# Kernel tuning notes

Hardware: AMD Instinct MI355X
Metric: run time of the kernel (lower is better)

Reference implementation:

```python
import jax, jax.numpy as jnp
import numpy as np

_SAMPLING_EPS = 1e-5


def setup_inputs() -> dict:
    key = jax.random.key(0)
    k1, k2, k3, k4, k5 = jax.random.split(key, 5)
    B, V = 128, 128000
    logits = jax.random.normal(k1, (B, V), dtype=jnp.float32)
    temperature = jax.random.uniform(k2, (B,), dtype=jnp.float32)  # some rows < eps -> greedy
    top_k = jax.random.randint(k3, (B,), 1, 64, dtype=jnp.int32)   # in [1, 63]
    top_p = jax.random.uniform(k4, (B,), dtype=jnp.float32, minval=0.05, maxval=1.0)
    noise_u = jax.random.uniform(k5, (B, V), dtype=jnp.float32, minval=1e-10, maxval=1.0)
    return {"logits": logits, "temperature": temperature, "top_k": top_k,
            "top_p": top_p, "noise_u": noise_u, "max_num_logprobs": 5}


def _apply_top_k_top_p(logits, k, p):
    # Faithful to vLLM: ascending sort, top-k threshold mask, top-p cumsum mask, scatter back.
    B, V = logits.shape
    order = jnp.argsort(logits, axis=-1)                       # ascending, [B, V]
    logits_sort = jnp.take_along_axis(logits, order, axis=-1)
    neg_inf = jnp.float32(-jnp.inf)
    # top-k: pivot value at position V - k; everything strictly below it -> -inf
    pivot_idx = (V - k.astype(jnp.int32))[:, None]             # [B, 1]
    pivot = jnp.take_along_axis(logits_sort, pivot_idx, axis=-1)
    logits_sort = jnp.where(logits_sort < pivot, neg_inf, logits_sort)
    # top-p: softmax over sorted logits, cumsum, drop prefix with mass <= 1 - p (keep last)
    probs_sort = jax.nn.softmax(logits_sort, axis=-1)
    probs_sum = jnp.cumsum(probs_sort, axis=-1)
    top_p_mask = probs_sum <= (1.0 - p)[:, None]
    top_p_mask = top_p_mask.at[:, -1].set(False)
    logits_sort = jnp.where(top_p_mask, neg_inf, logits_sort)
    # scatter back to original vocab order
    rows = jnp.arange(B)[:, None]
    return jnp.zeros_like(logits).at[rows, order].set(logits_sort)


def reference(logits, temperature, top_k, top_p, noise_u, max_num_logprobs):
    # temperature scaling (temp < eps means greedy; divide by 1.0 instead)
    temp = jnp.where(temperature < _SAMPLING_EPS, 1.0, temperature)
    logits = logits.astype(jnp.float32) / temp[:, None]
    # top-k / top-p filtering
    logits = _apply_top_k_top_p(logits, top_k, top_p)
    # probabilities and sampling
    probs = jax.nn.softmax(logits, axis=-1)
    greedy = jnp.argmax(probs, axis=-1)
    q = -jnp.log(noise_u)                                      # Exp(1) noise (q.exponential_())
    random = jnp.argmax(probs / q, axis=-1)
    sampled = jnp.where(temperature < _SAMPLING_EPS, greedy, random).astype(jnp.int32)
    # top-k logprobs
    logprobs = jax.nn.log_softmax(logits, axis=-1)
    topk_logprobs, topk_indices = jax.lax.top_k(logprobs, max_num_logprobs)
    return sampled, topk_indices.astype(jnp.int32), topk_logprobs
```

## Files before the change

### kernel.cpp

```cpp
#include <hip/hip_runtime.h>
#include <math.h>
#include <stdint.h>

#define BT     256
#define WPB    4
#define TOPC   64
#define CAPW   1024
#define WT     512
#define NSL_HI 16
#define NSL_LO 8
#define NC_MAX (NSL_HI * TOPC)

__device__ __forceinline__ unsigned f2ord(float f) {
    unsigned u = __float_as_uint(f);
    return u ^ ((u & 0x80000000u) ? 0xFFFFFFFFu : 0x80000000u);
}
__device__ __forceinline__ float ord2f(unsigned k) {
    unsigned u = (k & 0x80000000u) ? (k ^ 0x80000000u) : (k ^ 0xFFFFFFFFu);
    return __uint_as_float(u);
}

__device__ unsigned wave_rebuild64(unsigned* key, int* idx, unsigned n,
                                   int lane, unsigned* out_vst)
{
    unsigned kr[16]; int ir[16];
    #pragma unroll
    for (int g = 0; g < 16; ++g) {
        unsigned i = (unsigned)(g * 64 + lane);
        kr[g] = (i < n) ? key[i] : 0u;
        ir[g] = (i < n) ? idx[i] : 0;
    }
    unsigned p = 0u;
    for (int bit = 31; bit >= 0; --bit) {
        unsigned t = p | (1u << bit);
        int c = 0;
        #pragma unroll
        for (int g = 0; g < 16; ++g)
            c += __popcll(__ballot(kr[g] >= t));
        if (c >= TOPC) p = t;
    }
    const unsigned long long ltm = (1ull << lane) - 1ull;
    unsigned c = 0;
    #pragma unroll
    for (int g = 0; g < 16; ++g) {
        unsigned i = (unsigned)(g * 64 + lane);
        bool pa = (i < n) && (kr[g] > p);
        unsigned long long m = __ballot(pa);
        if (pa) { unsigned pos = c + (unsigned)__popcll(m & ltm); key[pos] = kr[g]; idx[pos] = ir[g]; }
        c += (unsigned)__popcll(m);
    }
    #pragma unroll
    for (int g = 0; g < 16; ++g) {
        unsigned i = (unsigned)(g * 64 + lane);
        bool pa = (i < n) && (kr[g] == p);
        unsigned long long m = __ballot(pa);
        if (pa) {
            unsigned pos = c + (unsigned)__popcll(m & ltm);
            if (pos < TOPC) { key[pos] = kr[g]; idx[pos] = ir[g]; }
        }
        c += (unsigned)__popcll(m);
    }
    *out_vst = p;
    return (c < TOPC) ? c : TOPC;
}

__global__ __launch_bounds__(BT) void phase1_topk_slices(
    const float* __restrict__ logits, uint2* __restrict__ cand,
    int V, int slice_len, int nsl)
{
    __shared__ unsigned s_key[WPB][CAPW];
    __shared__ int      s_idx[WPB][CAPW];

    const int row  = blockIdx.y;
    const int tid  = threadIdx.x;
    const int wid  = tid >> 6;
    const int lane = tid & 63;
    const int sl   = blockIdx.x * WPB + wid;
    const int s0   = sl * slice_len;
    int s_end = s0 + slice_len; if (s_end > V) s_end = V;
    const float* rowp = logits + (size_t)row * (size_t)V;
    unsigned* mykey = s_key[wid];
    int*      myidx = s_idx[wid];
    const unsigned long long ltm = (1ull << lane) - 1ull;

    const int  tb0 = s0 + lane * 8, tb1 = s0 + WT + lane * 8;
    const bool vt0 = tb0 < s_end,   vt1 = tb1 < s_end;
    float4 sa0 = {}, sb0 = {}, sa1 = {}, sb1 = {};
    if (vt0) { sa0 = *(const float4*)(rowp + tb0); sb0 = *(const float4*)(rowp + tb0 + 4); }
    if (vt1) { sa1 = *(const float4*)(rowp + tb1); sb1 = *(const float4*)(rowp + tb1 + 4); }

    const int t2 = s0 + 2 * WT, t3 = s0 + 3 * WT;
    const int pb0 = t2 + lane * 8, pb1 = t3 + lane * 8;
    bool pv0 = pb0 < s_end, pv1 = pb1 < s_end;
    float4 A0 = {}, B0 = {}, A1 = {}, B1 = {};
    if (pv0) { A0 = *(const float4*)(rowp + pb0); B0 = *(const float4*)(rowp + pb0 + 4); }
    if (pv1) { A1 = *(const float4*)(rowp + pb1); B1 = *(const float4*)(rowp + pb1 + 4); }

    unsigned k0[8], k1[8];
    if (vt0) {
        k0[0] = f2ord(sa0.x); k0[1] = f2ord(sa0.y); k0[2] = f2ord(sa0.z); k0[3] = f2ord(sa0.w);
        k0[4] = f2ord(sb0.x); k0[5] = f2ord(sb0.y); k0[6] = f2ord(sb0.z); k0[7] = f2ord(sb0.w);
    } else {
        #pragma unroll
        for (int j = 0; j < 8; ++j) k0[j] = 0u;
    }
    if (vt1) {
        k1[0] = f2ord(sa1.x); k1[1] = f2ord(sa1.y); k1[2] = f2ord(sa1.z); k1[3] = f2ord(sa1.w);
        k1[4] = f2ord(sb1.x); k1[5] = f2ord(sb1.y); k1[6] = f2ord(sb1.z); k1[7] = f2ord(sb1.w);
    } else {
        #pragma unroll
        for (int j = 0; j < 8; ++j) k1[j] = 0u;
    }

    unsigned lo = 0u, hi = 0xFFFFu;
    while (lo < hi) {
        unsigned mid = (lo + hi + 1u) >> 1;
        unsigned t = mid << 16;
        int cnt16 = 0;
        #pragma unroll
        for (int j = 0; j < 8; ++j) {
            cnt16 += __popcll(__ballot(k0[j] >= t));
            cnt16 += __popcll(__ballot(k1[j] >= t));
        }
        if (cnt16 >= TOPC) lo = mid; else hi = mid - 1u;
    }
    const unsigned thr = lo << 16;

    unsigned cnt = 0u;
    auto append8 = [&](const unsigned* k, int base, bool valid) {
        #pragma unroll
        for (int j = 0; j < 8; ++j) {
            bool pa = valid && (k[j] >= thr);
            unsigned long long m = __ballot(pa);
            if (pa) {
                unsigned pos = cnt + (unsigned)__popcll(m & ltm);
                if (pos < CAPW) { mykey[pos] = k[j]; myidx[pos] = base + j; }
            }
            cnt += (unsigned)__popcll(m);
        }
    };
    auto conv8 = [&](unsigned* k, const float4& a, const float4& b, bool valid) {
        if (valid) {
            k[0] = f2ord(a.x); k[1] = f2ord(a.y); k[2] = f2ord(a.z); k[3] = f2ord(a.w);
            k[4] = f2ord(b.x); k[5] = f2ord(b.y); k[6] = f2ord(b.z); k[7] = f2ord(b.w);
        } else {
            #pragma unroll
            for (int j = 0; j < 8; ++j) k[j] = 0u;
        }
    };

    append8(k0, tb0, vt0);
    append8(k1, tb1, vt1);

    for (int t = t2; t < s_end; t += WT) {
        float4 A2 = {}, B2 = {}; bool pv2 = false;
        int bn = t + 2 * WT + lane * 8;
        if (t + 2 * WT < s_end && bn < s_end) {
            A2 = *(const float4*)(rowp + bn); B2 = *(const float4*)(rowp + bn + 4);
            pv2 = true;
        }
        unsigned kk[8];
        conv8(kk, A0, B0, pv0);
        append8(kk, t + lane * 8, pv0);
        A0 = A1; B0 = B1; pv0 = pv1;
        A1 = A2; B1 = B2; pv1 = pv2;
    }

    asm volatile("s_waitcnt lgkmcnt(0)" ::: "memory");
    __builtin_amdgcn_sched_barrier(0);
    unsigned n = cnt;

    if (n > CAPW) {
        unsigned vst;
        cnt = wave_rebuild64(mykey, myidx, CAPW, lane, &vst);
        for (int t = s0; t < s_end; t += WT) {
            int bs = t + lane * 8;
            bool v = bs < s_end;
            float4 aa = {}, bb = {};
            if (v) { aa = *(const float4*)(rowp + bs); bb = *(const float4*)(rowp + bs + 4); }
            unsigned kk[8];
            conv8(kk, aa, bb, v);
            for (;;) {
                unsigned long long m[8]; unsigned tot = 0u;
                #pragma unroll
                for (int j = 0; j < 8; ++j) {
                    m[j] = __ballot(v && (kk[j] > vst));
                    tot += (unsigned)__popcll(m[j]);
                }
                if (cnt + tot <= CAPW) {
                    unsigned c2 = cnt;
                    #pragma unroll
                    for (int j = 0; j < 8; ++j) {
                        if (v && (kk[j] > vst)) {
                            unsigned pos = c2 + (unsigned)__popcll(m[j] & ltm);
                            mykey[pos] = kk[j]; myidx[pos] = bs + j;
                        }
                        c2 += (unsigned)__popcll(m[j]);
                    }
                    cnt = c2;
                    break;
                }
                asm volatile("s_waitcnt lgkmcnt(0)" ::: "memory");
                __builtin_amdgcn_sched_barrier(0);
                cnt = wave_rebuild64(mykey, myidx, cnt, lane, &vst);
            }
        }
        asm volatile("s_waitcnt lgkmcnt(0)" ::: "memory");
        __builtin_amdgcn_sched_barrier(0);
        n = cnt;
    }

    unsigned vfin;
    unsigned c2 = wave_rebuild64(mykey, myidx, n, lane, &vfin);
    asm volatile("s_waitcnt lgkmcnt(0)" ::: "memory");
    __builtin_amdgcn_sched_barrier(0);

    uint2* outp = cand + ((size_t)row * (unsigned)nsl + (unsigned)sl) * TOPC;
    unsigned e = (unsigned)lane;
    uint2 val = (e < c2) ? make_uint2(mykey[e], (unsigned)myidx[e])
                         : make_uint2(0u, 0u);
    outp[e] = val;
}

__device__ unsigned radix_select_compact4(uint2* s_buf, uint2* s_keep,
                                          unsigned (*s_hist)[16], unsigned* p_cnt2,
                                          unsigned n, int tid, int wid)
{
    unsigned prefix = 0u;
    int remaining = TOPC;
    for (int shift = 28; shift >= 0; shift -= 4) {
        if (tid < 64) ((unsigned*)s_hist)[tid] = 0u;
        __syncthreads();
        for (unsigned i = (unsigned)tid; i < n; i += BT) {
            unsigned k = s_buf[i].x;
            bool ing = (shift == 28) || ((k >> (shift + 4)) == (prefix >> (shift + 4)));
            if (ing) atomicAdd(&s_hist[wid][(k >> shift) & 15u], 1u);
        }
        __syncthreads();
        int cum = 0; int b = 0; unsigned hb = 0u;
        for (int bb = 15; bb >= 0; --bb) {
            unsigned h = s_hist[0][bb] + s_hist[1][bb] + s_hist[2][bb] + s_hist[3][bb];
            cum += (int)h;
            if (cum >= remaining) { b = bb; hb = h; break; }
        }
        remaining -= (cum - (int)hb);
        prefix |= ((unsigned)b) << shift;
        __syncthreads();
    }
    if (tid == 0) *p_cnt2 = 0u;
    __syncthreads();
    for (unsigned i = (unsigned)tid; i < n; i += BT) {
        uint2 c = s_buf[i];
        if (c.x > prefix) s_keep[atomicAdd(p_cnt2, 1u)] = c;
    }
    __syncthreads();
    for (unsigned i = (unsigned)tid; i < n; i += BT) {
        uint2 c = s_buf[i];
        if (c.x == prefix) {
            unsigned pos = atomicAdd(p_cnt2, 1u);
            if (pos < TOPC) s_keep[pos] = c;
        }
    }
    __syncthreads();
    return prefix;
}

__global__ __launch_bounds__(BT) void phase2_sample(
    const uint2* __restrict__ cand,
    const float* __restrict__ temperature,
    const int*   __restrict__ top_k,
    const float* __restrict__ top_p,
    const float* __restrict__ noise_u,
    float* __restrict__ out,
    int B, int V, int M, int nc)
{
    __shared__ uint2    s_buf[NC_MAX];
    __shared__ uint2    s_keep[TOPC];
    __shared__ unsigned s_hist[4][16];
    __shared__ unsigned s_cnt2;
    __shared__ float    sval[TOPC], se[TOPC], sq[TOPC];
    __shared__ int      sidx[TOPC];

    const int r   = blockIdx.x;
    const int tid = threadIdx.x;
    const int wid = tid >> 6;

    for (int i = tid; i < nc; i += BT)
        s_buf[i] = cand[(size_t)r * nc + i];
    __syncthreads();
    radix_select_compact4(s_buf, s_keep, s_hist, &s_cnt2, (unsigned)nc, tid, wid);

    for (int kk = 2; kk <= TOPC; kk <<= 1) {
        for (int j = kk >> 1; j > 0; j >>= 1) {
            if (tid < TOPC / 2) {
                int i0 = ((tid & ~(j - 1)) << 1) | (tid & (j - 1));
                int i1 = i0 | j;
                bool up = ((i0 & kk) == 0);
                uint2 A = s_keep[i0], Bv = s_keep[i1];
                bool gt = (A.x < Bv.x) || (A.x == Bv.x && A.y > Bv.y);
                if (gt == up) { s_keep[i0] = Bv; s_keep[i1] = A; }
            }
            __syncthreads();
        }
    }

    float temp_orig = temperature[r];
    float temp = (temp_orig < 1e-5f) ? 1.0f : temp_orig;

    if (tid < TOPC) {
        unsigned k = s_keep[tid].x;
        int id = (int)s_keep[tid].y;
        sval[tid] = ord2f(k) / temp;
        sidx[tid] = id;
        float u = noise_u[(size_t)r * (size_t)V + id];
        sq[tid] = -logf(u);
    }
    __syncthreads();
    if (tid < TOPC) se[tid] = expf(sval[tid] - sval[0]);
    __syncthreads();

    if (tid == 0) {
        int k = top_k[r];
        if (k < 1) k = 1; if (k > TOPC) k = TOPC;
        float p = top_p[r];

        float pivot = sval[k - 1];
        int m = k;
        while (m < TOPC && sval[m] >= pivot) ++m;

        float sum = 0.f;
        for (int i = 0; i < m; ++i) sum += se[i];

        float thr1 = 1.0f - p;
        float S = 0.f;
        int f = 1;
        for (int i = m - 1; i >= 1; --i) {
            S += se[i] / sum;
            if (S > thr1) { f = i + 1; break; }
        }

        float sum2 = 0.f;
        for (int i = 0; i < f; ++i) sum2 += se[i];

        int greedy = sidx[0];
        float best = -1.f; int bidx = 0x7fffffff;
        for (int i = 0; i < f; ++i) {
            float ratio = (se[i] / sum2) / sq[i];
            if (ratio > best || (ratio == best && sidx[i] < bidx)) {
                best = ratio; bidx = sidx[i];
            }
        }
        int sampled = (temp_orig < 1e-5f) ? greedy : bidx;

        float lse = logf(sum2);
        out[r] = (float)sampled;
        float* oidx = out + B + (size_t)r * M;
        float* olp  = out + B + (size_t)B * M + (size_t)r * M;
        int produced = 0;
        for (int i = 0; i < f && produced < M; ++i, ++produced) {
            oidx[produced] = (float)sidx[i];
            olp[produced]  = (sval[i] - sval[0]) - lse;
        }
        int v = 0;
        while (produced < M) {
            bool used = false;
            for (int i = 0; i < f; ++i) if (sidx[i] == v) { used = true; break; }
            if (!used) { oidx[produced] = (float)v; olp[produced] = -3.0e38f; ++produced; }
            ++v;
        }
    }
}

extern "C" void kernel_launch(void* const* d_in, const int* in_sizes, int n_in,
                              void* d_out, int out_size, void* d_ws, size_t ws_size,
                              hipStream_t stream)
{
    const float* logits      = (const float*)d_in[0];
    const float* temperature = (const float*)d_in[1];
    const int*   top_k       = (const int*)d_in[2];
    const float* top_p       = (const float*)d_in[3];
    const float* noise_u     = (const float*)d_in[4];

    const int B = in_sizes[1];
    const int V = in_sizes[0] / B;
    const int M = (out_size / B - 1) / 2;

    const size_t need16 = (size_t)B * NSL_HI * TOPC * sizeof(uint2);
    const int nsl = (ws_size >= need16) ? NSL_HI : NSL_LO;

    uint2* cand = (uint2*)d_ws;

    int slice_len = (((V + nsl - 1) / nsl) + 7) & ~7;

    dim3 g1(nsl / WPB, B);
    phase1_topk_slices<<<g1, BT, 0, stream>>>(logits, cand, V, slice_len, nsl);
    phase2_sample<<<B, BT, 0, stream>>>(cand, temperature, top_k, top_p, noise_u,
                                        (float*)d_out, B, V, M, nsl * TOPC);
}
```

Measured before the change: 177.4 us.

## Double vocab slices per row, prefetch deeper, size wave rebuild by count

Raises the number of vocabulary slices per row from 16 to 32, so each wave scans about 4000 elements and the grid has twice as many blocks. The slice scan now issues six tile loads up front with fixed unrolled stages in place of a rolling two-tile prefetch. The per-wave top-64 rebuild is templated on register count and picks a 4/8/16-group variant based on candidate count, cutting ballot work for small buffers. The cost is a phase-2 candidate pool twice as large (2048 per row) and a larger workspace requirement.

```diff
diff --git a/kernel.cpp b/kernel.cpp
--- a/kernel.cpp
+++ b/kernel.cpp
@@ -7,8 +7,8 @@
 #define TOPC   64
 #define CAPW   1024
 #define WT     512
-#define NSL_HI 16
-#define NSL_LO 8
+#define NSL_HI 32
+#define NSL_LO 16
 #define NC_MAX (NSL_HI * TOPC)
 
 __device__ __forceinline__ unsigned f2ord(float f) {
@@ -20,12 +20,13 @@
     return __uint_as_float(u);
 }
 
-__device__ unsigned wave_rebuild64(unsigned* key, int* idx, unsigned n,
-                                   int lane, unsigned* out_vst)
-{
-    unsigned kr[16]; int ir[16];
+template<int G>
+__device__ unsigned wave_rebuild64_g(unsigned* key, int* idx, unsigned n,
+                                     int lane, unsigned* out_vst)
+{
+    unsigned kr[G]; int ir[G];
     #pragma unroll
-    for (int g = 0; g < 16; ++g) {
+    for (int g = 0; g < G; ++g) {
         unsigned i = (unsigned)(g * 64 + lane);
         kr[g] = (i < n) ? key[i] : 0u;
         ir[g] = (i < n) ? idx[i] : 0;
@@ -35,14 +36,14 @@
         unsigned t = p | (1u << bit);
         int c = 0;
         #pragma unroll
-        for (int g = 0; g < 16; ++g)
+        for (int g = 0; g < G; ++g)
             c += __popcll(__ballot(kr[g] >= t));
         if (c >= TOPC) p = t;
     }
     const unsigned long long ltm = (1ull << lane) - 1ull;
     unsigned c = 0;
     #pragma unroll
-    for (int g = 0; g < 16; ++g) {
+    for (int g = 0; g < G; ++g) {
         unsigned i = (unsigned)(g * 64 + lane);
         bool pa = (i < n) && (kr[g] > p);
         unsigned long long m = __ballot(pa);
@@ -50,7 +51,7 @@
         c += (unsigned)__popcll(m);
     }
     #pragma unroll
-    for (int g = 0; g < 16; ++g) {
+    for (int g = 0; g < G; ++g) {
         unsigned i = (unsigned)(g * 64 + lane);
         bool pa = (i < n) && (kr[g] == p);
         unsigned long long m = __ballot(pa);
@@ -62,6 +63,15 @@
     }
     *out_vst = p;
     return (c < TOPC) ? c : TOPC;
+}
+
+__device__ __forceinline__ unsigned wave_rebuild64(unsigned* key, int* idx,
+                                                   unsigned n, int lane,
+                                                   unsigned* out_vst)
+{
+    if (n <= 256)  return wave_rebuild64_g<4>(key, idx, n, lane, out_vst);
+    if (n <= 512)  return wave_rebuild64_g<8>(key, idx, n, lane, out_vst);
+    return wave_rebuild64_g<16>(key, idx, n, lane, out_vst);
 }
 
 __global__ __launch_bounds__(BT) void phase1_topk_slices(
@@ -83,18 +93,24 @@
     int*      myidx = s_idx[wid];
     const unsigned long long ltm = (1ull << lane) - 1ull;
 
-    const int  tb0 = s0 + lane * 8, tb1 = s0 + WT + lane * 8;
-    const bool vt0 = tb0 < s_end,   vt1 = tb1 < s_end;
+    const int  tb0 = s0 + 0 * WT + lane * 8, tb1 = s0 + 1 * WT + lane * 8;
+    const int  tb2 = s0 + 2 * WT + lane * 8, tb3 = s0 + 3 * WT + lane * 8;
+    const int  tb4 = s0 + 4 * WT + lane * 8, tb5 = s0 + 5 * WT + lane * 8;
+    const int  tb6 = s0 + 6 * WT + lane * 8, tb7 = s0 + 7 * WT + lane * 8;
+    const bool vt0 = tb0 < s_end, vt1 = tb1 < s_end, vt2 = tb2 < s_end,
+               vt3 = tb3 < s_end, vt4 = tb4 < s_end, vt5 = tb5 < s_end,
+               vt6 = tb6 < s_end, vt7 = tb7 < s_end;
+
     float4 sa0 = {}, sb0 = {}, sa1 = {}, sb1 = {};
     if (vt0) { sa0 = *(const float4*)(rowp + tb0); sb0 = *(const float4*)(rowp + tb0 + 4); }
     if (vt1) { sa1 = *(const float4*)(rowp + tb1); sb1 = *(const float4*)(rowp + tb1 + 4); }
 
-    const int t2 = s0 + 2 * WT, t3 = s0 + 3 * WT;
-    const int pb0 = t2 + lane * 8, pb1 = t3 + lane * 8;
-    bool pv0 = pb0 < s_end, pv1 = pb1 < s_end;
-    float4 A0 = {}, B0 = {}, A1 = {}, B1 = {};
-    if (pv0) { A0 = *(const float4*)(rowp + pb0); B0 = *(const float4*)(rowp + pb0 + 4); }
-    if (pv1) { A1 = *(const float4*)(rowp + pb1); B1 = *(const float4*)(rowp + pb1 + 4); }
+    float4 A2 = {}, B2 = {}, A3 = {}, B3 = {};
+    float4 A4 = {}, B4 = {}, A5 = {}, B5 = {};
+    if (vt2) { A2 = *(const float4*)(rowp + tb2); B2 = *(const float4*)(rowp + tb2 + 4); }
+    if (vt3) { A3 = *(const float4*)(rowp + tb3); B3 = *(const float4*)(rowp + tb3 + 4); }
+    if (vt4) { A4 = *(const float4*)(rowp + tb4); B4 = *(const float4*)(rowp + tb4 + 4); }
+    if (vt5) { A5 = *(const float4*)(rowp + tb5); B5 = *(const float4*)(rowp + tb5 + 4); }
 
     unsigned k0[8], k1[8];
     if (vt0) {
@@ -152,18 +168,31 @@
     append8(k0, tb0, vt0);
     append8(k1, tb1, vt1);
 
-    for (int t = t2; t < s_end; t += WT) {
-        float4 A2 = {}, B2 = {}; bool pv2 = false;
-        int bn = t + 2 * WT + lane * 8;
-        if (t + 2 * WT < s_end && bn < s_end) {
-            A2 = *(const float4*)(rowp + bn); B2 = *(const float4*)(rowp + bn + 4);
-            pv2 = true;
-        }
+    {
         unsigned kk[8];
-        conv8(kk, A0, B0, pv0);
-        append8(kk, t + lane * 8, pv0);
-        A0 = A1; B0 = B1; pv0 = pv1;
-        A1 = A2; B1 = B2; pv1 = pv2;
+        conv8(kk, A2, B2, vt2);
+        if (vt6) { A2 = *(const float4*)(rowp + tb6); B2 = *(const float4*)(rowp + tb6 + 4); }
+        append8(kk, tb2, vt2);
+    }
+    {
+        unsigned kk[8];
+        conv8(kk, A3, B3, vt3);
+        if (vt7) { A3 = *(const float4*)(rowp + tb7); B3 = *(const float4*)(rowp + tb7 + 4); }
+        append8(kk, tb3, vt3);
+    }
+    {   unsigned kk[8]; conv8(kk, A4, B4, vt4); append8(kk, tb4, vt4); }
+    {   unsigned kk[8]; conv8(kk, A5, B5, vt5); append8(kk, tb5, vt5); }
+    {   unsigned kk[8]; conv8(kk, A2, B2, vt6); append8(kk, tb6, vt6); }
+    {   unsigned kk[8]; conv8(kk, A3, B3, vt7); append8(kk, tb7, vt7); }
+
+    for (int t = s0 + 8 * WT; t < s_end; t += WT) {
+        int bs = t + lane * 8;
+        bool v = bs < s_end;
+        float4 aa = {}, bb = {};
+        if (v) { aa = *(const float4*)(rowp + bs); bb = *(const float4*)(rowp + bs + 4); }
+        unsigned kk[8];
+        conv8(kk, aa, bb, v);
+        append8(kk, bs, v);
     }
 
     asm volatile("s_waitcnt lgkmcnt(0)" ::: "memory");
@@ -172,7 +201,7 @@
 
     if (n > CAPW) {
         unsigned vst;
-        cnt = wave_rebuild64(mykey, myidx, CAPW, lane, &vst);
+        cnt = wave_rebuild64_g<16>(mykey, myidx, CAPW, lane, &vst);
         for (int t = s0; t < s_end; t += WT) {
             int bs = t + lane * 8;
             bool v = bs < s_end;
@@ -202,7 +231,7 @@
                 }
                 asm volatile("s_waitcnt lgkmcnt(0)" ::: "memory");
                 __builtin_amdgcn_sched_barrier(0);
-                cnt = wave_rebuild64(mykey, myidx, cnt, lane, &vst);
+                cnt = wave_rebuild64_g<16>(mykey, myidx, cnt, lane, &vst);
             }
         }
         asm volatile("s_waitcnt lgkmcnt(0)" ::: "memory");
@@ -385,8 +414,8 @@
     const int V = in_sizes[0] / B;
     const int M = (out_size / B - 1) / 2;
 
-    const size_t need16 = (size_t)B * NSL_HI * TOPC * sizeof(uint2);
-    const int nsl = (ws_size >= need16) ? NSL_HI : NSL_LO;
+    const size_t need32 = (size_t)B * NSL_HI * TOPC * sizeof(uint2);
+    const int nsl = (ws_size >= need32) ? NSL_HI : NSL_LO;
 
     uint2* cand = (uint2*)d_ws;
 
```

Measured after the change: 180.0 us. About the same (+1.4%).

## Restructure phase-1 top-k into more blocks with sampled row threshold and in-block merge

Applied to the files above, without the earlier changes.

Replaces the per-slice wave top-64 kernel with a finer-grained grid (16 tiles of 512 per block, about 16 blocks per row) so more blocks cover the logits read. Each wave derives a conservative threshold from a 2048-element sample at the start of the row, compares raw floats against it, and appends survivors to a smaller per-wave buffer. The four wave results are merged in-block by radix select so each block emits 64 candidates. This raises parallelism and cuts shared-memory use. The cost is an extra redundant sample read per block and an extra two-pass rescan if a wave overflows.

```diff
diff --git a/kernel.cpp b/kernel.cpp
--- a/kernel.cpp
+++ b/kernel.cpp
@@ -3,13 +3,12 @@
 #include <stdint.h>
 
 #define BT     256
-#define WPB    4
 #define TOPC   64
-#define CAPW   1024
-#define WT     512
-#define NSL_HI 16
-#define NSL_LO 8
-#define NC_MAX (NSL_HI * TOPC)
+#define FT     512
+#define SAMP   2048
+#define CAPWV  576
+#define GW     9
+#define CAPF   2048
 
 __device__ __forceinline__ unsigned f2ord(float f) {
     unsigned u = __float_as_uint(f);
@@ -20,12 +19,13 @@
     return __uint_as_float(u);
 }
 
-__device__ unsigned wave_rebuild64(unsigned* key, int* idx, unsigned n,
-                                   int lane, unsigned* out_vst)
-{
-    unsigned kr[16]; int ir[16];
+template<int G>
+__device__ unsigned wave_rebuild64_g(unsigned* key, int* idx, unsigned n,
+                                     int lane, unsigned* out_vst)
+{
+    unsigned kr[G]; int ir[G];
     #pragma unroll
-    for (int g = 0; g < 16; ++g) {
+    for (int g = 0; g < G; ++g) {
         unsigned i = (unsigned)(g * 64 + lane);
         kr[g] = (i < n) ? key[i] : 0u;
         ir[g] = (i < n) ? idx[i] : 0;
@@ -35,14 +35,14 @@
         unsigned t = p | (1u << bit);
         int c = 0;
         #pragma unroll
-        for (int g = 0; g < 16; ++g)
+        for (int g = 0; g < G; ++g)
             c += __popcll(__ballot(kr[g] >= t));
         if (c >= TOPC) p = t;
     }
     const unsigned long long ltm = (1ull << lane) - 1ull;
     unsigned c = 0;
     #pragma unroll
-    for (int g = 0; g < 16; ++g) {
+    for (int g = 0; g < G; ++g) {
         unsigned i = (unsigned)(g * 64 + lane);
         bool pa = (i < n) && (kr[g] > p);
         unsigned long long m = __ballot(pa);
@@ -50,7 +50,7 @@
         c += (unsigned)__popcll(m);
     }
     #pragma unroll
-    for (int g = 0; g < 16; ++g) {
+    for (int g = 0; g < G; ++g) {
         unsigned i = (unsigned)(g * 64 + lane);
         bool pa = (i < n) && (kr[g] == p);
         unsigned long long m = __ballot(pa);
@@ -62,164 +62,6 @@
     }
     *out_vst = p;
     return (c < TOPC) ? c : TOPC;
-}
-
-__global__ __launch_bounds__(BT) void phase1_topk_slices(
-    const float* __restrict__ logits, uint2* __restrict__ cand,
-    int V, int slice_len, int nsl)
-{
-    __shared__ unsigned s_key[WPB][CAPW];
-    __shared__ int      s_idx[WPB][CAPW];
-
-    const int row  = blockIdx.y;
-    const int tid  = threadIdx.x;
-    const int wid  = tid >> 6;
-    const int lane = tid & 63;
-    const int sl   = blockIdx.x * WPB + wid;
-    const int s0   = sl * slice_len;
-    int s_end = s0 + slice_len; if (s_end > V) s_end = V;
-    const float* rowp = logits + (size_t)row * (size_t)V;
-    unsigned* mykey = s_key[wid];
-    int*      myidx = s_idx[wid];
-    const unsigned long long ltm = (1ull << lane) - 1ull;
-
-    const int  tb0 = s0 + lane * 8, tb1 = s0 + WT + lane * 8;
-    const bool vt0 = tb0 < s_end,   vt1 = tb1 < s_end;
-    float4 sa0 = {}, sb0 = {}, sa1 = {}, sb1 = {};
-    if (vt0) { sa0 = *(const float4*)(rowp + tb0); sb0 = *(const float4*)(rowp + tb0 + 4); }
-    if (vt1) { sa1 = *(const float4*)(rowp + tb1); sb1 = *(const float4*)(rowp + tb1 + 4); }
-
-    const int t2 = s0 + 2 * WT, t3 = s0 + 3 * WT;
-    const int pb0 = t2 + lane * 8, pb1 = t3 + lane * 8;
-    bool pv0 = pb0 < s_end, pv1 = pb1 < s_end;
-    float4 A0 = {}, B0 = {}, A1 = {}, B1 = {};
-    if (pv0) { A0 = *(const float4*)(rowp + pb0); B0 = *(const float4*)(rowp + pb0 + 4); }
-    if (pv1) { A1 = *(const float4*)(rowp + pb1); B1 = *(const float4*)(rowp + pb1 + 4); }
-
-    unsigned k0[8], k1[8];
-    if (vt0) {
-        k0[0] = f2ord(sa0.x); k0[1] = f2ord(sa0.y); k0[2] = f2ord(sa0.z); k0[3] = f2ord(sa0.w);
-        k0[4] = f2ord(sb0.x); k0[5] = f2ord(sb0.y); k0[6] = f2ord(sb0.z); k0[7] = f2ord(sb0.w);
-    } else {
-        #pragma unroll
-        for (int j = 0; j < 8; ++j) k0[j] = 0u;
-    }
-    if (vt1) {
-        k1[0] = f2ord(sa1.x); k1[1] = f2ord(sa1.y); k1[2] = f2ord(sa1.z); k1[3] = f2ord(sa1.w);
-        k1[4] = f2ord(sb1.x); k1[5] = f2ord(sb1.y); k1[6] = f2ord(sb1.z); k1[7] = f2ord(sb1.w);
-    } else {
-        #pragma unroll
-        for (int j = 0; j < 8; ++j) k1[j] = 0u;
-    }
-
-    unsigned lo = 0u, hi = 0xFFFFu;
-    while (lo < hi) {
-        unsigned mid = (lo + hi + 1u) >> 1;
-        unsigned t = mid << 16;
-        int cnt16 = 0;
-        #pragma unroll
-        for (int j = 0; j < 8; ++j) {
-            cnt16 += __popcll(__ballot(k0[j] >= t));
-            cnt16 += __popcll(__ballot(k1[j] >= t));
-        }
-        if (cnt16 >= TOPC) lo = mid; else hi = mid - 1u;
-    }
-    const unsigned thr = lo << 16;
-
-    unsigned cnt = 0u;
-    auto append8 = [&](const unsigned* k, int base, bool valid) {
-        #pragma unroll
-        for (int j = 0; j < 8; ++j) {
-            bool pa = valid && (k[j] >= thr);
-            unsigned long long m = __ballot(pa);
-            if (pa) {
-                unsigned pos = cnt + (unsigned)__popcll(m & ltm);
-                if (pos < CAPW) { mykey[pos] = k[j]; myidx[pos] = base + j; }
-            }
-            cnt += (unsigned)__popcll(m);
-        }
-    };
-    auto conv8 = [&](unsigned* k, const float4& a, const float4& b, bool valid) {
-        if (valid) {
-            k[0] = f2ord(a.x); k[1] = f2ord(a.y); k[2] = f2ord(a.z); k[3] = f2ord(a.w);
-            k[4] = f2ord(b.x); k[5] = f2ord(b.y); k[6] = f2ord(b.z); k[7] = f2ord(b.w);
-        } else {
-            #pragma unroll
-            for (int j = 0; j < 8; ++j) k[j] = 0u;
-        }
-    };
-
-    append8(k0, tb0, vt0);
-    append8(k1, tb1, vt1);
-
-    for (int t = t2; t < s_end; t += WT) {
-        float4 A2 = {}, B2 = {}; bool pv2 = false;
-        int bn = t + 2 * WT + lane * 8;
-        if (t + 2 * WT < s_end && bn < s_end) {
-            A2 = *(const float4*)(rowp + bn); B2 = *(const float4*)(rowp + bn + 4);
-            pv2 = true;
-        }
-        unsigned kk[8];
-        conv8(kk, A0, B0, pv0);
-        append8(kk, t + lane * 8, pv0);
-        A0 = A1; B0 = B1; pv0 = pv1;
-        A1 = A2; B1 = B2; pv1 = pv2;
-    }
-
-    asm volatile("s_waitcnt lgkmcnt(0)" ::: "memory");
-    __builtin_amdgcn_sched_barrier(0);
-    unsigned n = cnt;
-
-    if (n > CAPW) {
-        unsigned vst;
-        cnt = wave_rebuild64(mykey, myidx, CAPW, lane, &vst);
-        for (int t = s0; t < s_end; t += WT) {
-            int bs = t + lane * 8;
-            bool v = bs < s_end;
-            float4 aa = {}, bb = {};
-            if (v) { aa = *(const float4*)(rowp + bs); bb = *(const float4*)(rowp + bs + 4); }
-            unsigned kk[8];
-            conv8(kk, aa, bb, v);
-            for (;;) {
-                unsigned long long m[8]; unsigned tot = 0u;
-                #pragma unroll
-                for (int j = 0; j < 8; ++j) {
-                    m[j] = __ballot(v && (kk[j] > vst));
-                    tot += (unsigned)__popcll(m[j]);
-                }
-                if (cnt + tot <= CAPW) {
-                    unsigned c2 = cnt;
-                    #pragma unroll
-                    for (int j = 0; j < 8; ++j) {
-                        if (v && (kk[j] > vst)) {
-                            unsigned pos = c2 + (unsigned)__popcll(m[j] & ltm);
-                            mykey[pos] = kk[j]; myidx[pos] = bs + j;
-                        }
-                        c2 += (unsigned)__popcll(m[j]);
-                    }
-                    cnt = c2;
-                    break;
-                }
-                asm volatile("s_waitcnt lgkmcnt(0)" ::: "memory");
-                __builtin_amdgcn_sched_barrier(0);
-                cnt = wave_rebuild64(mykey, myidx, cnt, lane, &vst);
-            }
-        }
-        asm volatile("s_waitcnt lgkmcnt(0)" ::: "memory");
-        __builtin_amdgcn_sched_barrier(0);
-        n = cnt;
-    }
-
-    unsigned vfin;
-    unsigned c2 = wave_rebuild64(mykey, myidx, n, lane, &vfin);
-    asm volatile("s_waitcnt lgkmcnt(0)" ::: "memory");
-    __builtin_amdgcn_sched_barrier(0);
-
-    uint2* outp = cand + ((size_t)row * (unsigned)nsl + (unsigned)sl) * TOPC;
-    unsigned e = (unsigned)lane;
-    uint2 val = (e < c2) ? make_uint2(mykey[e], (unsigned)myidx[e])
-                         : make_uint2(0u, 0u);
-    outp[e] = val;
 }
 
 __device__ unsigned radix_select_compact4(uint2* s_buf, uint2* s_keep,
@@ -265,7 +107,130 @@
     return prefix;
 }
 
-__global__ __launch_bounds__(BT) void phase2_sample(
+__global__ __launch_bounds__(BT) void block_topk(
+    const float* __restrict__ logits, uint2* __restrict__ cand,
+    int V, int tpr, int tpb, int bpr)
+{
+    __shared__ unsigned s_key[4][CAPWV];
+    __shared__ int      s_idx[4][CAPWV];
+    __shared__ uint2    s_all[4 * TOPC];
+    __shared__ uint2    s_keep[TOPC];
+    __shared__ unsigned s_hist[4][16];
+    __shared__ unsigned s_cnt2;
+
+    const int row  = blockIdx.y;
+    const int bx   = blockIdx.x;
+    const int tid  = threadIdx.x;
+    const int wid  = tid >> 6;
+    const int lane = tid & 63;
+    const unsigned long long ltm = (1ull << lane) - 1ull;
+    const float* rowp = logits + (size_t)row * (size_t)V;
+    unsigned* mykey = s_key[wid];
+    int*      myidx = s_idx[wid];
+
+    unsigned kr[SAMP / 64];
+    #pragma unroll
+    for (int g = 0; g < SAMP / FT; ++g) {
+        int c0 = g * FT + lane * 8;
+        if (c0 + 8 <= V) {
+            float4 a = *(const float4*)(rowp + c0);
+            float4 b = *(const float4*)(rowp + c0 + 4);
+            kr[g*8+0] = f2ord(a.x); kr[g*8+1] = f2ord(a.y);
+            kr[g*8+2] = f2ord(a.z); kr[g*8+3] = f2ord(a.w);
+            kr[g*8+4] = f2ord(b.x); kr[g*8+5] = f2ord(b.y);
+            kr[g*8+6] = f2ord(b.z); kr[g*8+7] = f2ord(b.w);
+        } else {
+            #pragma unroll
+            for (int j = 0; j < 8; ++j) kr[g*8+j] = 0u;
+        }
+    }
+    unsigned lo = 0u, hi = 0xFFFFu;
+    while (lo < hi) {
+        unsigned mid = (lo + hi + 1u) >> 1;
+        unsigned t = mid << 16;
+        int c = 0;
+        #pragma unroll
+        for (int j = 0; j < SAMP / 64; ++j) c += __popcll(__ballot(kr[j] >= t));
+        if (c >= TOPC) lo = mid; else hi = mid - 1u;
+    }
+    const unsigned thr = lo << 16;
+    const float thr_f = ord2f(thr);
+
+    const int tpw = tpb >> 2;
+    const int tw0 = bx * tpb + wid * tpw;
+    int tw1 = tw0 + tpw; if (tw1 > tpr) tw1 = tpr;
+    unsigned cnt = 0u;
+    for (int t = tw0; t < tw1; ++t) {
+        const int base = t * FT + lane * 8;
+        const bool v = (base + 8 <= V);
+        float4 a = {}, b = {};
+        if (v) { a = *(const float4*)(rowp + base); b = *(const float4*)(rowp + base + 4); }
+        float f[8] = {a.x, a.y, a.z, a.w, b.x, b.y, b.z, b.w};
+        #pragma unroll
+        for (int j = 0; j < 8; ++j) {
+            bool pa = v && (f[j] >= thr_f);
+            unsigned long long m = __ballot(pa);
+            if (pa) {
+                unsigned pos = cnt + (unsigned)__popcll(m & ltm);
+                if (pos < CAPWV) { mykey[pos] = f2ord(f[j]); myidx[pos] = base + j; }
+            }
+            cnt += (unsigned)__popcll(m);
+        }
+    }
+
+    if (cnt > CAPWV) {
+        unsigned vst;
+        (void)wave_rebuild64_g<GW>(mykey, myidx, CAPWV, lane, &vst);
+        cnt = 0u;
+        for (int t = tw0; t < tw1; ++t) {
+            const int base = t * FT + lane * 8;
+            const bool v = (base + 8 <= V);
+            float4 a = {}, b = {};
+            if (v) { a = *(const float4*)(rowp + base); b = *(const float4*)(rowp + base + 4); }
+            float f[8] = {a.x, a.y, a.z, a.w, b.x, b.y, b.z, b.w};
+            #pragma unroll
+            for (int j = 0; j < 8; ++j) {
+                bool pa = v && (f2ord(f[j]) > vst);
+                unsigned long long m = __ballot(pa);
+                if (pa) {
+                    unsigned pos = cnt + (unsigned)__popcll(m & ltm);
+                    if (pos < CAPWV) { mykey[pos] = f2ord(f[j]); myidx[pos] = base + j; }
+                }
+                cnt += (unsigned)__popcll(m);
+            }
+        }
+        for (int t = tw0; t < tw1; ++t) {
+            const int base = t * FT + lane * 8;
+            const bool v = (base + 8 <= V);
+            float4 a = {}, b = {};
+            if (v) { a = *(const float4*)(rowp + base); b = *(const float4*)(rowp + base + 4); }
+            float f[8] = {a.x, a.y, a.z, a.w, b.x, b.y, b.z, b.w};
+            #pragma unroll
+            for (int j = 0; j < 8; ++j) {
+                bool pa = v && (f2ord(f[j]) == vst);
+                unsigned long long m = __ballot(pa);
+                if (pa) {
+                    unsigned pos = cnt + (unsigned)__popcll(m & ltm);
+                    if (pos < CAPWV) { mykey[pos] = vst; myidx[pos] = base + j; }
+                }
+                cnt += (unsigned)__popcll(m);
+            }
+        }
+    }
+
+    unsigned vfin;
+    unsigned c2 = wave_rebuild64_g<GW>(mykey, myidx,
+                                       (cnt < CAPWV ? cnt : CAPWV), lane, &vfin);
+    s_all[wid * TOPC + lane] = ((unsigned)lane < c2)
+        ? make_uint2(mykey[lane], (unsigned)myidx[lane])
+        : make_uint2(0u, 0u);
+    __syncthreads();
+    radix_select_compact4(s_all, s_keep, s_hist, &s_cnt2, 4u * TOPC, tid, wid);
+    if (tid < TOPC)
+        cand[((size_t)row * (unsigned)bpr + (unsigned)bx) * TOPC + tid] = s_keep[tid];
+}
+
+__global__ __launch_bounds__(BT) void phase2_final(
     const uint2* __restrict__ cand,
     const float* __restrict__ temperature,
     const int*   __restrict__ top_k,
@@ -274,7 +239,7 @@
     float* __restrict__ out,
     int B, int V, int M, int nc)
 {
-    __shared__ uint2    s_buf[NC_MAX];
+    __shared__ uint2    s_buf[CAPF];
     __shared__ uint2    s_keep[TOPC];
     __shared__ unsigned s_hist[4][16];
     __shared__ unsigned s_cnt2;
@@ -286,7 +251,7 @@
     const int wid = tid >> 6;
 
     for (int i = tid; i < nc; i += BT)
-        s_buf[i] = cand[(size_t)r * nc + i];
+        s_buf[i] = cand[(size_t)r * (unsigned)nc + i];
     __syncthreads();
     radix_select_compact4(s_buf, s_keep, s_hist, &s_cnt2, (unsigned)nc, tid, wid);
 
@@ -385,15 +350,20 @@
     const int V = in_sizes[0] / B;
     const int M = (out_size / B - 1) / 2;
 
-    const size_t need16 = (size_t)B * NSL_HI * TOPC * sizeof(uint2);
-    const int nsl = (ws_size >= need16) ? NSL_HI : NSL_LO;
+    const int tpr = (V + FT - 1) / FT;
+
+    int tpb = 16;
+    int bpr = (tpr + tpb - 1) / tpb;
+    while ((bpr * TOPC > CAPF ||
+            (size_t)B * bpr * TOPC * sizeof(uint2) > ws_size) && bpr > 1) {
+        tpb += 4;
+        bpr = (tpr + tpb - 1) / tpb;
+    }
 
     uint2* cand = (uint2*)d_ws;
 
-    int slice_len = (((V + nsl - 1) / nsl) + 7) & ~7;
-
-    dim3 g1(nsl / WPB, B);
-    phase1_topk_slices<<<g1, BT, 0, stream>>>(logits, cand, V, slice_len, nsl);
-    phase2_sample<<<B, BT, 0, stream>>>(cand, temperature, top_k, top_p, noise_u,
-                                        (float*)d_out, B, V, M, nsl * TOPC);
-}
+    dim3 g1(bpr, B);
+    block_topk<<<g1, BT, 0, stream>>>(logits, cand, V, tpr, tpb, bpr);
+    phase2_final<<<B, BT, 0, stream>>>(cand, temperature, top_k, top_p, noise_u,
+                                       (float*)d_out, B, V, M, bpr * TOPC);
+}
```

New measurement: 198.8 us. 12.0% more time.
